# Performance work log

Measured on AMD Instinct MI355X. Metric: run time of the kernel, lower is better.

Reference implementation:

```python
import jax, jax.numpy as jnp
import numpy as np

B, S, D_MODEL, N_HEADS, D_FEAT = 8, 1024, 1024, 16, 64


def setup_inputs() -> dict:
    key = jax.random.key(0)
    ks = jax.random.split(key, 5)
    sin = jax.random.normal(ks[0], (B, S, D_MODEL), dtype=jnp.float32)
    mask = jnp.ones((B, S), dtype=bool)  # only its presence matters in the original
    # Per-head Linear(d_model -> d_feature): weight stored as [H, d_model, d_feature]
    lim = 1.0 / np.sqrt(D_MODEL)
    Wx = jax.random.uniform(ks[1], (N_HEADS, D_MODEL, D_FEAT), dtype=jnp.float32, minval=-lim, maxval=lim)
    bx = jax.random.uniform(ks[2], (N_HEADS, D_FEAT), dtype=jnp.float32, minval=-lim, maxval=lim)
    # Output projection Linear(H*d_feature -> d_model), stored as [in, out]
    lim_p = 1.0 / np.sqrt(N_HEADS * D_FEAT)
    Wp = jax.random.uniform(ks[3], (N_HEADS * D_FEAT, D_MODEL), dtype=jnp.float32, minval=-lim_p, maxval=lim_p)
    bp = jax.random.uniform(ks[4], (D_MODEL,), dtype=jnp.float32, minval=-lim_p, maxval=lim_p)
    return {"sin": sin, "mask": mask, "Wx": Wx, "bx": bx, "Wp": Wp, "bp": bp}


def reference(sin, mask, Wx, bx, Wp, bp):
    # All heads batched: per-head linear projection  [B,H,S,F]
    x = jnp.einsum("bsd,hdf->bhsf", sin, Wx) + bx[None, :, None, :]
    # Cosine-similarity scores: x x^T / (||x|| ||x||^T)  -> [B,H,S,S]
    norm = jnp.sqrt(jnp.sum(x * x, axis=-1, keepdims=True))  # [B,H,S,1]
    scores = jnp.einsum("bhsf,bhtf->bhst", x, x) / (norm * jnp.swapaxes(norm, -2, -1))
    # Original quirk: when mask is not None, entries that are exactly 0.0 get -inf
    scores = jnp.where(scores == 0.0, -jnp.inf, scores)
    p_attn = jax.nn.softmax(scores, axis=-1)
    out = jnp.einsum("bhst,bhtf->bhsf", p_attn, x)
    # Concat heads: [B,S,H*F]
    out = jnp.transpose(out, (0, 2, 1, 3)).reshape(out.shape[0], out.shape[2], -1)
    return out @ Wp + bp
```

## Files before the change

kernel.cpp:

```cpp
#include <hip/hip_runtime.h>
#include <hip/hip_bf16.h>
#include <math.h>

typedef _Float16 f16;
typedef _Float16 half8 __attribute__((ext_vector_type(8)));
typedef float f32x4 __attribute__((ext_vector_type(4)));
typedef float f32x16 __attribute__((ext_vector_type(16)));
typedef unsigned int u32;

#define NB 8
#define NS 1024
#define DM 1024
#define NH 16
#define NF 64

__global__ __launch_bounds__(256) void csin_kernel(const float* __restrict__ in, f16* __restrict__ out) {
  long gid = (long)blockIdx.x * 256 + threadIdx.x;
  const float4* p = (const float4*)(in + gid * 8);
  float4 a = p[0], b = p[1];
  half8 v;
  v[0] = (f16)a.x; v[1] = (f16)a.y; v[2] = (f16)a.z; v[3] = (f16)a.w;
  v[4] = (f16)b.x; v[5] = (f16)b.y; v[6] = (f16)b.z; v[7] = (f16)b.w;
  *(half8*)(out + gid * 8) = v;
}

__global__ __launch_bounds__(256) void cwx_kernel(const float* __restrict__ Wx, f16* __restrict__ W2T) {
  __shared__ float T[64][65];
  int h = blockIdx.x >> 4, d0 = (blockIdx.x & 15) * 64;
  int tid = threadIdx.x;
  const float* src = Wx + ((size_t)h * 1024 + d0) * 64;
  int row = tid >> 2, cg = (tid & 3) * 16;
#pragma unroll
  for (int k = 0; k < 4; ++k) {
    float4 v = *(const float4*)(src + (size_t)row * 64 + cg + k * 4);
    T[row][cg + k * 4 + 0] = v.x;
    T[row][cg + k * 4 + 1] = v.y;
    T[row][cg + k * 4 + 2] = v.z;
    T[row][cg + k * 4 + 3] = v.w;
  }
  __syncthreads();
  int f = tid >> 2, dg = (tid & 3) * 16;
  f16 o[16];
#pragma unroll
  for (int j = 0; j < 16; ++j) o[j] = (f16)T[dg + j][f];
  *(half8*)(W2T + (size_t)(h * 64 + f) * DM + d0 + dg) = *(half8*)&o[0];
  *(half8*)(W2T + (size_t)(h * 64 + f) * DM + d0 + dg + 8) = *(half8*)&o[8];
}

__global__ __launch_bounds__(256) void cwp_kernel(const float* __restrict__ Wp, f16* __restrict__ WpT) {
  __shared__ float T[64][65];
  int n0 = (blockIdx.x >> 4) * 64, d0 = (blockIdx.x & 15) * 64;
  int tid = threadIdx.x;
  int row = tid >> 2, cg = (tid & 3) * 16;
#pragma unroll
  for (int k = 0; k < 4; ++k) {
    float4 v = *(const float4*)(Wp + (size_t)(d0 + row) * DM + n0 + cg + k * 4);
    T[row][cg + k * 4 + 0] = v.x;
    T[row][cg + k * 4 + 1] = v.y;
    T[row][cg + k * 4 + 2] = v.z;
    T[row][cg + k * 4 + 3] = v.w;
  }
  __syncthreads();
  int f = tid >> 2, dg = (tid & 3) * 16;
  f16 o[16];
#pragma unroll
  for (int j = 0; j < 16; ++j) o[j] = (f16)T[dg + j][f];
  *(half8*)(WpT + (size_t)(n0 + f) * DM + d0 + dg) = *(half8*)&o[0];
  *(half8*)(WpT + (size_t)(n0 + f) * DM + d0 + dg + 8) = *(half8*)&o[8];
}

template <int MODE>
__global__ __launch_bounds__(256) void gemm_kernel(const f16* __restrict__ A, const f16* __restrict__ Bt,
                                                   const float* __restrict__ bias, void* __restrict__ Cv) {
  __shared__ f16 As[128][64];
  __shared__ f16 Bs[128][64];
  int tid = threadIdx.x;
  int l = tid & 63, wv = tid >> 6;
  int wm = wv >> 1, wn = wv & 1;
  int xcd = blockIdx.x & 7, m = blockIdx.x >> 3;
  int bm = ((m >> 3) << 3) | xcd;
  int bn = m & 7;
  int lr = l & 15, lh = l >> 4;

  f32x4 acc[4][4];
#pragma unroll
  for (int i = 0; i < 4; ++i)
#pragma unroll
    for (int j = 0; j < 4; ++j) acc[i][j] = (f32x4)0.f;

  const f16* gA = A + (size_t)(bm * 128 + wv * 32 + (l >> 3)) * DM + (l & 7) * 8;
  const f16* gB = Bt + (size_t)(bn * 128 + wv * 32 + (l >> 3)) * DM + (l & 7) * 8;
  f16* ldsA = &As[wv * 32][0];
  f16* ldsB = &Bs[wv * 32][0];

  for (int k0 = 0; k0 < DM; k0 += 64) {
    __syncthreads();
#pragma unroll
    for (int c = 0; c < 4; ++c) {
      __builtin_amdgcn_global_load_lds(
          (const __attribute__((address_space(1))) void*)(gA + k0 + (size_t)c * 8 * DM),
          (__attribute__((address_space(3))) void*)(ldsA + c * 512), 16, 0, 0);
      __builtin_amdgcn_global_load_lds(
          (const __attribute__((address_space(1))) void*)(gB + k0 + (size_t)c * 8 * DM),
          (__attribute__((address_space(3))) void*)(ldsB + c * 512), 16, 0, 0);
    }
    __syncthreads();
#pragma unroll
    for (int ks = 0; ks < 2; ++ks) {
      half8 af[4], bf[4];
#pragma unroll
      for (int mi = 0; mi < 4; ++mi) af[mi] = *(const half8*)&As[wm * 64 + mi * 16 + lr][ks * 32 + lh * 8];
#pragma unroll
      for (int ni = 0; ni < 4; ++ni) bf[ni] = *(const half8*)&Bs[wn * 64 + ni * 16 + lr][ks * 32 + lh * 8];
#pragma unroll
      for (int mi = 0; mi < 4; ++mi)
#pragma unroll
        for (int ni = 0; ni < 4; ++ni)
          acc[mi][ni] = __builtin_amdgcn_mfma_f32_16x16x32_f16(af[mi], bf[ni], acc[mi][ni], 0, 0, 0);
    }
  }

#pragma unroll
  for (int mi = 0; mi < 4; ++mi)
#pragma unroll
    for (int ni = 0; ni < 4; ++ni) {
      int gc = bn * 128 + wn * 64 + ni * 16 + lr;
      float bv = bias[gc];
#pragma unroll
      for (int r = 0; r < 4; ++r) {
        int gr = bm * 128 + wm * 64 + mi * 16 + lh * 4 + r;
        float v = acc[mi][ni][r] + bv;
        if (MODE == 0) {
          f16* x = (f16*)Cv;
          int b = gr >> 10, s = gr & 1023, h = gc >> 6, f = gc & 63;
          x[(size_t)((b * NH + h) * NS + s) * NF + f] = (f16)v;
        } else {
          ((float*)Cv)[(size_t)gr * DM + gc] = v;
        }
      }
    }
}

__global__ __launch_bounds__(256) void transnorm_kernel(f16* __restrict__ x, f16* __restrict__ xT) {
  __shared__ f16 T[64][64];
  __shared__ float sinv[64];
  int bh = blockIdx.x >> 4, s0 = (blockIdx.x & 15) * 64;
  int tid = threadIdx.x;
  f16* xb = x + (size_t)bh * (NS * NF);
  half8 vv[2];
#pragma unroll
  for (int it = 0; it < 2; ++it) {
    int idx = it * 256 + tid;
    int sr = idx >> 3, fcb = idx & 7;
    half8 v = *(const half8*)(xb + (size_t)(s0 + sr) * NF + fcb * 8);
    vv[it] = v;
    *(half8*)&T[sr][((fcb ^ ((sr >> 3) & 7)) * 8)] = v;
    float s = 0.f;
#pragma unroll
    for (int j = 0; j < 8; ++j) {
      float u = (float)v[j];
      s += u * u;
    }
    s += __shfl_xor(s, 1, 64);
    s += __shfl_xor(s, 2, 64);
    s += __shfl_xor(s, 4, 64);
    if ((tid & 7) == 0) sinv[sr] = rsqrtf(s);
  }
  __syncthreads();
#pragma unroll
  for (int it = 0; it < 2; ++it) {
    int idx = it * 256 + tid;
    int fr = idx >> 3, scb = idx & 7;
    half8 v;
#pragma unroll
    for (int j = 0; j < 8; ++j) v[j] = T[scb * 8 + j][(((fr >> 3) ^ scb) * 8) + (fr & 7)];
    *(half8*)(xT + ((size_t)bh * NF + fr) * NS + s0 + scb * 8) = v;
  }
#pragma unroll
  for (int it = 0; it < 2; ++it) {
    int idx = it * 256 + tid;
    int sr = idx >> 3, fcb = idx & 7;
    float inv = sinv[sr];
    half8 v = vv[it], o;
#pragma unroll
    for (int j = 0; j < 8; ++j) o[j] = (f16)((float)v[j] * inv);
    *(half8*)(xb + (size_t)(s0 + sr) * NF + fcb * 8) = o;
  }
}

__global__ __launch_bounds__(256) void attn_kernel(const f16* __restrict__ xn, const f16* __restrict__ xT,
                                                   f16* __restrict__ ao) {
  int tid = threadIdx.x;
  int l = tid & 63, wv = tid >> 6;
  int lq = l & 31, hi = l >> 5;
  int kq = hi * 8;
  int xcd = blockIdx.x & 7, m = blockIdx.x >> 3;
  int bh = ((m >> 2) << 3) | xcd;
  int q0 = (m & 3) * 256;
  const f16* xnb = xn + (size_t)bh * (NS * NF);
  const f16* xTb = xT + (size_t)bh * (NF * NS);

  half8 bq[2][4];
#pragma unroll
  for (int qs = 0; qs < 2; ++qs)
#pragma unroll
    for (int ks = 0; ks < 4; ++ks)
      bq[qs][ks] = *(const half8*)(xnb + (size_t)(q0 + wv * 64 + qs * 32 + lq) * NF + ks * 16 + kq);

  f32x16 accO[2][2];
  accO[0][0] = (f32x16)0.f;
  accO[0][1] = (f32x16)0.f;
  accO[1][0] = (f32x16)0.f;
  accO[1][1] = (f32x16)0.f;
  float rs[2] = {0.f, 0.f};

  for (int t0 = 0; t0 < NS; t0 += 128) {
#pragma unroll
    for (int ti = 0; ti < 4; ++ti) {
      half8 ak[4];
      int tr = t0 + ti * 32 + lq;
#pragma unroll
      for (int ks = 0; ks < 4; ++ks)
        ak[ks] = *(const half8*)(xnb + (size_t)tr * NF + ks * 16 + kq);
      half8 vbl[2][2];
#pragma unroll
      for (int sub = 0; sub < 2; ++sub)
#pragma unroll
        for (int ni = 0; ni < 2; ++ni)
          vbl[sub][ni] = *(const half8*)(xTb + (size_t)(ni * 32 + lq) * NS + t0 + ti * 32 + sub * 16 + kq);

#pragma unroll
      for (int qs = 0; qs < 2; ++qs) {
        f32x16 sa = (f32x16)0.f;
#pragma unroll
        for (int ks = 0; ks < 4; ++ks)
          sa = __builtin_amdgcn_mfma_f32_32x32x16_f16(ak[ks], bq[qs][ks], sa, 0, 0, 0);

        u32 pk[8];
#pragma unroll
        for (int mm = 0; mm < 8; ++mm) {
          float a = sa[2 * mm], b = sa[2 * mm + 1];
          float ea = (a == 0.f) ? 0.f : __expf(a - 1.f);
          float eb = (b == 0.f) ? 0.f : __expf(b - 1.f);
          rs[qs] += ea + eb;
          auto h = __builtin_amdgcn_cvt_pkrtz(ea, eb);
          pk[mm] = __builtin_bit_cast(u32, h);
        }
        u32 sw[8];
#pragma unroll
        for (int mm = 0; mm < 8; ++mm) sw[mm] = (u32)__shfl_xor((int)pk[mm], 32, 64);
        bool lo = (hi == 0);
        uint4 a0, a1;
        a0.x = lo ? pk[0] : sw[2];
        a0.y = lo ? pk[1] : sw[3];
        a0.z = lo ? sw[0] : pk[2];
        a0.w = lo ? sw[1] : pk[3];
        a1.x = lo ? pk[4] : sw[6];
        a1.y = lo ? pk[5] : sw[7];
        a1.z = lo ? sw[4] : pk[6];
        a1.w = lo ? sw[5] : pk[7];
        half8 pa0 = __builtin_bit_cast(half8, a0);
        half8 pa1 = __builtin_bit_cast(half8, a1);
#pragma unroll
        for (int sub = 0; sub < 2; ++sub) {
          half8 pa = sub ? pa1 : pa0;
#pragma unroll
          for (int ni = 0; ni < 2; ++ni)
            accO[qs][ni] = __builtin_amdgcn_mfma_f32_32x32x16_f16(pa, vbl[sub][ni], accO[qs][ni], 0, 0, 0);
        }
      }
    }
  }

  rs[0] += __shfl_xor(rs[0], 32, 64);
  rs[1] += __shfl_xor(rs[1], 32, 64);

  int b = bh >> 4, h = bh & 15;
#pragma unroll
  for (int qs = 0; qs < 2; ++qs)
#pragma unroll
    for (int r = 0; r < 16; ++r) {
      int qoff = (r & 3) + 8 * (r >> 2) + 4 * hi;
      float rv = __shfl(rs[qs], qoff, 64);
      float rinv = 1.0f / rv;
      int qg = q0 + wv * 64 + qs * 32 + qoff;
#pragma unroll
      for (int ni = 0; ni < 2; ++ni) {
        int f = ni * 32 + lq;
        ao[((size_t)(b * NS + qg)) * DM + h * NF + f] = (f16)(accO[qs][ni][r] * rinv);
      }
    }
}

extern "C" void kernel_launch(void* const* d_in, const int* in_sizes, int n_in,
                              void* d_out, int out_size, void* d_ws, size_t ws_size,
                              hipStream_t stream) {
  const float* sin_in = (const float*)d_in[0];
  const float* Wx = (const float*)d_in[2];
  const float* bx = (const float*)d_in[3];
  const float* Wp = (const float*)d_in[4];
  const float* bp = (const float*)d_in[5];
  float* out = (float*)d_out;

  char* p = (char*)d_ws;
  f16* sinb = (f16*)p;                      p += (size_t)NB * NS * DM * 2;
  f16* x    = (f16*)p;                      p += (size_t)NB * NH * NS * NF * 2;
  f16* xT   = (f16*)p;                      p += (size_t)NB * NH * NF * NS * 2;
  f16* W2T  = (f16*)p;                      p += (size_t)DM * DM * 2;
  f16* WpT  = (f16*)p;                      p += (size_t)DM * DM * 2;
  f16* ao   = sinb;

  csin_kernel<<<4096, 256, 0, stream>>>(sin_in, sinb);
  cwx_kernel<<<256, 256, 0, stream>>>(Wx, W2T);
  cwp_kernel<<<256, 256, 0, stream>>>(Wp, WpT);
  gemm_kernel<0><<<512, 256, 0, stream>>>(sinb, W2T, bx, (void*)x);
  transnorm_kernel<<<2048, 256, 0, stream>>>(x, xT);
  attn_kernel<<<512, 256, 0, stream>>>(x, xT, ao);
  gemm_kernel<1><<<512, 256, 0, stream>>>(ao, WpT, bp, (void*)out);
}
```

Before: 243.1 us.

## Stage K/V tiles through double-buffered LDS with async global_load_lds

```diff
diff --git a/kernel.cpp b/kernel.cpp
--- a/kernel.cpp
+++ b/kernel.cpp
@@ -190,6 +190,9 @@
 
 __global__ __launch_bounds__(256) void attn_kernel(const f16* __restrict__ xn, const f16* __restrict__ xT,
                                                    f16* __restrict__ ao) {
+  __shared__ f16 KB[2][2048];
+  __shared__ f16 VB[2][2048];
+
   int tid = threadIdx.x;
   int l = tid & 63, wv = tid >> 6;
   int lq = l & 31, hi = l >> 5;
@@ -200,6 +203,23 @@
   const f16* xnb = xn + (size_t)bh * (NS * NF);
   const f16* xTb = xT + (size_t)bh * (NF * NS);
 
+  int krow = wv * 8 + (l >> 3);
+  const f16* gK0 = xnb + (size_t)krow * NF + (((l & 7) ^ (krow & 7)) * 8);
+  int vrow = wv * 16 + (l >> 2);
+  const f16* gV0 = xTb + (size_t)vrow * NS + (((l & 3) ^ (vrow & 3)) * 8);
+
+  int akoff[4], vboff[2][2];
+#pragma unroll
+  for (int ks = 0; ks < 4; ++ks)
+    akoff[ks] = lq * 128 + ((((ks * 2 + hi)) ^ (lq & 7)) << 4);
+#pragma unroll
+  for (int sub = 0; sub < 2; ++sub)
+#pragma unroll
+    for (int ni = 0; ni < 2; ++ni) {
+      int r = ni * 32 + lq;
+      vboff[sub][ni] = r * 64 + (((sub * 2 + hi) ^ (r & 3)) << 4);
+    }
+
   half8 bq[2][4];
 #pragma unroll
   for (int qs = 0; qs < 2; ++qs)
@@ -214,43 +234,74 @@
   accO[1][1] = (f32x16)0.f;
   float rs[2] = {0.f, 0.f};
 
-  for (int t0 = 0; t0 < NS; t0 += 128) {
-#pragma unroll
-    for (int ti = 0; ti < 4; ++ti) {
-      half8 ak[4];
-      int tr = t0 + ti * 32 + lq;
+#define STAGE(buf, t0_)                                                                              \
+  do {                                                                                               \
+    __builtin_amdgcn_global_load_lds(                                                                \
+        (const __attribute__((address_space(1))) void*)(gK0 + (size_t)(t0_) * NF),                   \
+        (__attribute__((address_space(3))) void*)(&KB[buf][wv * 512]), 16, 0, 0);                    \
+    __builtin_amdgcn_global_load_lds(                                                                \
+        (const __attribute__((address_space(1))) void*)(gV0 + (t0_)),                                \
+        (__attribute__((address_space(3))) void*)(&VB[buf][wv * 512]), 16, 0, 0);                    \
+  } while (0)
+
+  const float L2E = 1.4426950408889634f;
+
+  STAGE(0, 0);
+  asm volatile("s_waitcnt vmcnt(0)" ::: "memory");
+  __syncthreads();
+
+  int cur = 0;
+  for (int t = 0; t < 32; ++t) {
+    if (t < 31) STAGE(cur ^ 1, (t + 1) * 32);
+
+    const char* kb = (const char*)&KB[cur][0];
+    const char* vb = (const char*)&VB[cur][0];
+    half8 ak[4];
+#pragma unroll
+    for (int ks = 0; ks < 4; ++ks) ak[ks] = *(const half8*)(kb + akoff[ks]);
+    half8 vbl[2][2];
+#pragma unroll
+    for (int sub = 0; sub < 2; ++sub)
+#pragma unroll
+      for (int ni = 0; ni < 2; ++ni) vbl[sub][ni] = *(const half8*)(vb + vboff[sub][ni]);
+
+#pragma unroll
+    for (int qs = 0; qs < 2; ++qs) {
+      f32x16 sa = (f32x16)0.f;
+      __builtin_amdgcn_s_setprio(1);
 #pragma unroll
       for (int ks = 0; ks < 4; ++ks)
-        ak[ks] = *(const half8*)(xnb + (size_t)tr * NF + ks * 16 + kq);
-      half8 vbl[2][2];
-#pragma unroll
-      for (int sub = 0; sub < 2; ++sub)
-#pragma unroll
-        for (int ni = 0; ni < 2; ++ni)
-          vbl[sub][ni] = *(const half8*)(xTb + (size_t)(ni * 32 + lq) * NS + t0 + ti * 32 + sub * 16 + kq);
-
-#pragma unroll
-      for (int qs = 0; qs < 2; ++qs) {
-        f32x16 sa = (f32x16)0.f;
-#pragma unroll
-        for (int ks = 0; ks < 4; ++ks)
-          sa = __builtin_amdgcn_mfma_f32_32x32x16_f16(ak[ks], bq[qs][ks], sa, 0, 0, 0);
-
-        u32 pk[8];
-#pragma unroll
-        for (int mm = 0; mm < 8; ++mm) {
-          float a = sa[2 * mm], b = sa[2 * mm + 1];
-          float ea = (a == 0.f) ? 0.f : __expf(a - 1.f);
-          float eb = (b == 0.f) ? 0.f : __expf(b - 1.f);
-          rs[qs] += ea + eb;
-          auto h = __builtin_amdgcn_cvt_pkrtz(ea, eb);
-          pk[mm] = __builtin_bit_cast(u32, h);
-        }
+        sa = __builtin_amdgcn_mfma_f32_32x32x16_f16(ak[ks], bq[qs][ks], sa, 0, 0, 0);
+      __builtin_amdgcn_s_setprio(0);
+
+      u32 pk[8];
+#pragma unroll
+      for (int mm = 0; mm < 8; ++mm) {
+        float a = sa[2 * mm], b = sa[2 * mm + 1];
+        float ea = (a == 0.f) ? 0.f : exp2f(__builtin_fmaf(a, L2E, -L2E));
+        float eb = (b == 0.f) ? 0.f : exp2f(__builtin_fmaf(b, L2E, -L2E));
+        rs[qs] += ea + eb;
+        auto h = __builtin_amdgcn_cvt_pkrtz(ea, eb);
+        pk[mm] = __builtin_bit_cast(u32, h);
+      }
+      uint4 a0, a1;
+#if __has_builtin(__builtin_amdgcn_permlane32_swap)
+      {
+        auto s02 = __builtin_amdgcn_permlane32_swap((int)pk[0], (int)pk[2], false, false);
+        auto s13 = __builtin_amdgcn_permlane32_swap((int)pk[1], (int)pk[3], false, false);
+        auto s46 = __builtin_amdgcn_permlane32_swap((int)pk[4], (int)pk[6], false, false);
+        auto s57 = __builtin_amdgcn_permlane32_swap((int)pk[5], (int)pk[7], false, false);
+        a0.x = (u32)s02[0]; a0.z = (u32)s02[1];
+        a0.y = (u32)s13[0]; a0.w = (u32)s13[1];
+        a1.x = (u32)s46[0]; a1.z = (u32)s46[1];
+        a1.y = (u32)s57[0]; a1.w = (u32)s57[1];
+      }
+#else
+      {
         u32 sw[8];
 #pragma unroll
         for (int mm = 0; mm < 8; ++mm) sw[mm] = (u32)__shfl_xor((int)pk[mm], 32, 64);
         bool lo = (hi == 0);
-        uint4 a0, a1;
         a0.x = lo ? pk[0] : sw[2];
         a0.y = lo ? pk[1] : sw[3];
         a0.z = lo ? sw[0] : pk[2];
@@ -259,18 +310,26 @@
         a1.y = lo ? pk[5] : sw[7];
         a1.z = lo ? sw[4] : pk[6];
         a1.w = lo ? sw[5] : pk[7];
-        half8 pa0 = __builtin_bit_cast(half8, a0);
-        half8 pa1 = __builtin_bit_cast(half8, a1);
-#pragma unroll
-        for (int sub = 0; sub < 2; ++sub) {
-          half8 pa = sub ? pa1 : pa0;
-#pragma unroll
-          for (int ni = 0; ni < 2; ++ni)
-            accO[qs][ni] = __builtin_amdgcn_mfma_f32_32x32x16_f16(pa, vbl[sub][ni], accO[qs][ni], 0, 0, 0);
-        }
-      }
-    }
-  }
+      }
+#endif
+      half8 pa0 = __builtin_bit_cast(half8, a0);
+      half8 pa1 = __builtin_bit_cast(half8, a1);
+      __builtin_amdgcn_s_setprio(1);
+#pragma unroll
+      for (int sub = 0; sub < 2; ++sub) {
+        half8 pa = sub ? pa1 : pa0;
+#pragma unroll
+        for (int ni = 0; ni < 2; ++ni)
+          accO[qs][ni] = __builtin_amdgcn_mfma_f32_32x32x16_f16(pa, vbl[sub][ni], accO[qs][ni], 0, 0, 0);
+      }
+      __builtin_amdgcn_s_setprio(0);
+    }
+
+    asm volatile("s_waitcnt vmcnt(0)" ::: "memory");
+    __syncthreads();
+    cur ^= 1;
+  }
+#undef STAGE
 
   rs[0] += __shfl_xor(rs[0], 32, 64);
   rs[1] += __shfl_xor(rs[1], 32, 64);
```

New measurement: 237.0 us. 2.5% less time.
